# Performance work log

Hardware: AMD Instinct MI355X
Metric: run time of the kernel (lower is better)

The kernel has to match this reference:

```python
import jax, jax.numpy as jnp
import numpy as np

N = 65536   # collocation points
D = 2       # input dim
C = 16      # num subdomains / partitions (4x4 grid)
PH = 128    # PoU hidden dim
PNMID = 2   # PoU middle (residual) layers: depth=4 -> 2 middle
SW = 256    # subnet width
SNMID = 2   # subnet middle layers: eqx MLP depth=3 -> 2 width->width layers


def setup_inputs() -> dict:
    key = jax.random.key(0)
    ks = jax.random.split(key, 8)

    def w(k, shape, fan_in):
        return jax.random.normal(k, shape, jnp.float32) / jnp.sqrt(jnp.float32(fan_in))

    x = jax.random.uniform(ks[0], (N, D), jnp.float32)  # points in [0,1]^2
    # 4x4 grid of axis-aligned subdomains covering [0,1]^2
    g = np.linspace(0.0, 1.0, 5)
    lo = np.stack(np.meshgrid(g[:-1], g[:-1], indexing='ij'), -1).reshape(-1, 2)
    hi = np.stack(np.meshgrid(g[1:], g[1:], indexing='ij'), -1).reshape(-1, 2)
    centers = jnp.asarray((lo + hi) / 2.0, jnp.float32)  # [C, D]
    scales = jnp.asarray((hi - lo) / 2.0, jnp.float32)   # [C, D]

    return dict(
        x=x, centers=centers, scales=scales,
        pou_W0=w(ks[1], (D, PH), D), pou_b0=jnp.zeros((PH,), jnp.float32),
        pou_Wmid=w(ks[2], (PNMID, PH, PH), PH), pou_bmid=jnp.zeros((PNMID, PH), jnp.float32),
        pou_Wl=w(ks[3], (PH, C), PH), pou_bl=jnp.zeros((C,), jnp.float32),
        sub_W0=w(ks[4], (C, D, SW), D), sub_b0=jnp.zeros((C, SW), jnp.float32),
        sub_Wmid=w(ks[5], (C, SNMID, SW, SW), SW), sub_bmid=jnp.zeros((C, SNMID, SW), jnp.float32),
        sub_Wl=w(ks[6], (C, SW, 1), SW), sub_bl=jnp.zeros((C, 1), jnp.float32),
    )


def reference(x, centers, scales,
              pou_W0, pou_b0, pou_Wmid, pou_bmid, pou_Wl, pou_bl,
              sub_W0, sub_b0, sub_Wmid, sub_bmid, sub_Wl, sub_bl):
    # --- PoU gating net: residual ReLU MLP + softmax over partitions ---
    h = jax.nn.relu(x @ pou_W0 + pou_b0)                  # [N, PH]
    for l in range(pou_Wmid.shape[0]):
        h = h + jax.nn.relu(h @ pou_Wmid[l] + pou_bmid[l])
    wgt = jax.nn.softmax(h @ pou_Wl + pou_bl, axis=-1)    # [N, C] window weights

    # --- per-subdomain input normalization + batched subnet MLPs (tanh) ---
    xn = (x[None, :, :] - centers[:, None, :]) / scales[:, None, :]  # [C, N, D]
    g = jnp.tanh(jnp.einsum('cnd,cdw->cnw', xn, sub_W0) + sub_b0[:, None, :])  # [C, N, SW]
    for l in range(sub_Wmid.shape[1]):
        g = jnp.tanh(jnp.einsum('cnw,cwv->cnv', g, sub_Wmid[:, l]) + sub_bmid[:, l][:, None, :])
    u = (jnp.einsum('cnw,cwo->cno', g, sub_Wl) + sub_bl[:, None, :])[:, :, 0]  # [C, N]

    # --- windowed weighted sum:  acc_n = sum_c w[n,c] * u[c,n] ---
    acc = jnp.einsum('nc,cn->n', wgt, u)                  # [N]

    # --- ansatz: hard Dirichlet BC on the unit box: u = acc * prod_d x_d (1-x_d) ---
    return acc * jnp.prod(x * (1.0 - x), axis=-1)
```

## Files before the change

### kernel.cpp

```cpp
#include <hip/hip_runtime.h>

#define NPTS 65536
#define CC 16
#define PH 128
#define SW 256
#define MB 64
#define SP 264
#define TS 2.8853900817779268f

typedef _Float16 half8 __attribute__((ext_vector_type(8)));
typedef _Float16 half4 __attribute__((ext_vector_type(4)));
typedef _Float16 half2 __attribute__((ext_vector_type(2)));
typedef float float4_ __attribute__((ext_vector_type(4)));
typedef float float2_ __attribute__((ext_vector_type(2)));
typedef unsigned int uint2_ __attribute__((ext_vector_type(2)));

__device__ __forceinline__ float tanh_e(float y) {
    float e = __builtin_amdgcn_exp2f(y);
    float r = __builtin_amdgcn_rcpf(e + 1.0f);
    return fmaf(-2.0f, r, 1.0f);
}

__device__ __forceinline__ void store_pk4(_Float16* p, float a, float b, float c, float d) {
    uint2_ u;
    u.x = __builtin_bit_cast(unsigned int, __builtin_amdgcn_cvt_pkrtz(a, b));
    u.y = __builtin_bit_cast(unsigned int, __builtin_amdgcn_cvt_pkrtz(c, d));
    *(uint2_*)p = u;
}

__global__ __launch_bounds__(256) void prep_wt(const float* __restrict__ Wmid,
                                               _Float16* __restrict__ Wt) {
    __shared__ float T[64][65];
    int b = blockIdx.x;
    int cl = b >> 4;
    int tile = b & 15;
    int w0 = (tile >> 2) * 64, v0 = (tile & 3) * 64;
    int t = threadIdx.x;
    int col = t & 63, row4 = t >> 6;
    const float* src = Wmid + ((size_t)cl << 16);
#pragma unroll
    for (int rr = 0; rr < 16; ++rr) {
        int wl = rr * 4 + row4;
        T[wl][col] = src[(size_t)(w0 + wl) * 256 + v0 + col];
    }
    __syncthreads();
    _Float16* dst = Wt + ((size_t)cl << 16);
#pragma unroll
    for (int rr = 0; rr < 16; ++rr) {
        int v = rr * 4 + row4;
        dst[(size_t)(v0 + v) * 256 + w0 + col] = (_Float16)(T[col][v] * TS);
    }
}

__global__ __launch_bounds__(256) void pou_kernel(
    const float* __restrict__ x, const float* __restrict__ W0,
    const float* __restrict__ b0, const float* __restrict__ Wmid,
    const float* __restrict__ bmid, const float* __restrict__ Wl,
    const float* __restrict__ bl, float* __restrict__ wgtT) {
    __shared__ float hA[64][PH + 1];
    int t = threadIdx.x;
    int p = t & 63;
    int g4 = __builtin_amdgcn_readfirstlane(t >> 6);
    int jb = g4 * 32;
    int n0 = blockIdx.x * 64;
    float x0 = x[(size_t)(n0 + p) * 2];
    float x1 = x[(size_t)(n0 + p) * 2 + 1];

#pragma unroll
    for (int jj = 0; jj < 32; ++jj) {
        int j = jb + jj;
        float a = x0 * W0[j] + x1 * W0[PH + j] + b0[j];
        hA[p][j] = a > 0.f ? a : 0.f;
    }
    __syncthreads();

    for (int l = 0; l < 2; ++l) {
        float acc[32];
#pragma unroll
        for (int jj = 0; jj < 32; ++jj) acc[jj] = bmid[l * PH + jb + jj];
        for (int k = 0; k < PH; ++k) {
            float hv = hA[p][k];
#pragma unroll
            for (int jj = 0; jj < 32; ++jj)
                acc[jj] += hv * Wmid[(l * PH + k) * PH + jb + jj];
        }
        float resv[32];
#pragma unroll
        for (int jj = 0; jj < 32; ++jj) resv[jj] = hA[p][jb + jj];
        __syncthreads();
#pragma unroll
        for (int jj = 0; jj < 32; ++jj) {
            float r = acc[jj] > 0.f ? acc[jj] : 0.f;
            hA[p][jb + jj] = resv[jj] + r;
        }
        __syncthreads();
    }

    int c4 = g4 * 4;
    float lacc[4];
#pragma unroll
    for (int cc = 0; cc < 4; ++cc) lacc[cc] = bl[c4 + cc];
    for (int k = 0; k < PH; ++k) {
        float hv = hA[p][k];
#pragma unroll
        for (int cc = 0; cc < 4; ++cc) lacc[cc] += hv * Wl[k * CC + c4 + cc];
    }
    __syncthreads();
#pragma unroll
    for (int cc = 0; cc < 4; ++cc) hA[p][c4 + cc] = lacc[cc];
    __syncthreads();

    if (t < 64) {
        float lg[CC];
#pragma unroll
        for (int c = 0; c < CC; ++c) lg[c] = hA[t][c];
        float m = lg[0];
#pragma unroll
        for (int c = 1; c < CC; ++c) m = fmaxf(m, lg[c]);
        float s = 0.f;
#pragma unroll
        for (int c = 0; c < CC; ++c) {
            lg[c] = __builtin_amdgcn_exp2f((lg[c] - m) * 1.4426950408889634f);
            s += lg[c];
        }
        float inv = 1.0f / s;
#pragma unroll
        for (int c = 0; c < CC; ++c)
            wgtT[(size_t)c * NPTS + n0 + t] = lg[c] * inv;
    }
}

__global__ __launch_bounds__(256, 4) void subnet_kernel(
    const float* __restrict__ x, const float* __restrict__ centers,
    const float* __restrict__ scales, const float* __restrict__ W0,
    const float* __restrict__ b0, const _Float16* __restrict__ Wt,
    const float* __restrict__ bmid, const float* __restrict__ Wl,
    const float* __restrict__ bl, const float* __restrict__ wgtT,
    float* __restrict__ out) {
    __shared__ _Float16 g[MB * SP];
    __shared__ float part[4][MB];
    int t = threadIdx.x;
    int c = blockIdx.y;
    int n0 = blockIdx.x * MB;

    {
        float cx0 = centers[c * 2], cx1 = centers[c * 2 + 1];
        float is0 = 1.0f / scales[c * 2], is1 = 1.0f / scales[c * 2 + 1];
        int ln = t & 63;
        int pb = (t >> 6) * 16;
        const float* W0c = W0 + (size_t)c * 2 * SW;
        float4_ w0 = *(const float4_*)&W0c[ln * 4];
        float4_ w1 = *(const float4_*)&W0c[SW + ln * 4];
        float4_ bb = *(const float4_*)&b0[c * SW + ln * 4];
        w0 *= TS; w1 *= TS; bb *= TS;
#pragma unroll 4
        for (int p = 0; p < 16; ++p) {
            float2_ xv = *(const float2_*)&x[(size_t)(n0 + pb + p) * 2];
            float xn0 = (xv[0] - cx0) * is0;
            float xn1 = (xv[1] - cx1) * is1;
            float tv[4];
#pragma unroll
            for (int j = 0; j < 4; ++j)
                tv[j] = tanh_e(fmaf(xn0, w0[j], fmaf(xn1, w1[j], bb[j])));
            store_pk4(&g[(pb + p) * SP + ln * 4], tv[0], tv[1], tv[2], tv[3]);
        }
    }
    __syncthreads();

    int lane = t & 63;
    int wave = t >> 6;
    int quad = lane >> 4;
    int l16 = lane & 15;
    int mb = wave * 64;

    {
        const _Float16* Wp = Wt + (((size_t)(c * 2 + 0)) << 16);
        const _Float16* Arow = Wp + (mb + l16) * SW + quad * 8;
        const float* bp = bmid + (c * 2 + 0) * SW + mb + quad * 4;
        float4_ acc[4][4];
#pragma unroll
        for (int mt = 0; mt < 4; ++mt) {
            float4_ bv = *(const float4_*)&bp[mt * 16];
            bv *= TS;
#pragma unroll
            for (int nt = 0; nt < 4; ++nt) acc[mt][nt] = bv;
        }
        __builtin_amdgcn_s_setprio(1);
#pragma unroll
        for (int kt = 0; kt < 8; ++kt) {
            half8 a[4], b[4];
#pragma unroll
            for (int mt = 0; mt < 4; ++mt)
                a[mt] = *(const half8*)&Arow[mt * 16 * SW + kt * 32];
#pragma unroll
            for (int nt = 0; nt < 4; ++nt)
                b[nt] = *(const half8*)&g[(nt * 16 + l16) * SP + kt * 32 + quad * 8];
#pragma unroll
            for (int mt = 0; mt < 4; ++mt)
#pragma unroll
                for (int nt = 0; nt < 4; ++nt)
                    acc[mt][nt] = __builtin_amdgcn_mfma_f32_16x16x32_f16(
                        a[mt], b[nt], acc[mt][nt], 0, 0, 0);
        }
        __builtin_amdgcn_s_setprio(0);
#pragma unroll
        for (int mt = 0; mt < 4; ++mt)
#pragma unroll
            for (int nt = 0; nt < 4; ++nt) {
                acc[mt][nt][0] = tanh_e(acc[mt][nt][0]);
                acc[mt][nt][1] = tanh_e(acc[mt][nt][1]);
                acc[mt][nt][2] = tanh_e(acc[mt][nt][2]);
                acc[mt][nt][3] = tanh_e(acc[mt][nt][3]);
            }
        __syncthreads();
#pragma unroll
        for (int mt = 0; mt < 4; ++mt) {
#pragma unroll
            for (int nt = 0; nt < 4; ++nt) {
                store_pk4(&g[(nt * 16 + l16) * SP + mb + mt * 16 + quad * 4],
                          acc[mt][nt][0], acc[mt][nt][1],
                          acc[mt][nt][2], acc[mt][nt][3]);
            }
        }
        __syncthreads();
    }

    {
        const _Float16* Wp = Wt + (((size_t)(c * 2 + 1)) << 16);
        const _Float16* Arow = Wp + (mb + l16) * SW + quad * 8;
        const float* bp = bmid + (c * 2 + 1) * SW + mb + quad * 4;
        float4_ acc[4][4];
#pragma unroll
        for (int mt = 0; mt < 4; ++mt) {
            float4_ bv = *(const float4_*)&bp[mt * 16];
            bv *= TS;
#pragma unroll
            for (int nt = 0; nt < 4; ++nt) acc[mt][nt] = bv;
        }
        __builtin_amdgcn_s_setprio(1);
#pragma unroll
        for (int kt = 0; kt < 8; ++kt) {
            half8 a[4], b[4];
#pragma unroll
            for (int mt = 0; mt < 4; ++mt)
                a[mt] = *(const half8*)&Arow[mt * 16 * SW + kt * 32];
#pragma unroll
            for (int nt = 0; nt < 4; ++nt)
                b[nt] = *(const half8*)&g[(nt * 16 + l16) * SP + kt * 32 + quad * 8];
#pragma unroll
            for (int mt = 0; mt < 4; ++mt)
#pragma unroll
                for (int nt = 0; nt < 4; ++nt)
                    acc[mt][nt] = __builtin_amdgcn_mfma_f32_16x16x32_f16(
                        a[mt], b[nt], acc[mt][nt], 0, 0, 0);
        }
        __builtin_amdgcn_s_setprio(0);
        const float* wlp = Wl + c * SW + mb + quad * 4;
        float s[4] = {0.f, 0.f, 0.f, 0.f};
#pragma unroll
        for (int mt = 0; mt < 4; ++mt) {
            float4_ wv = *(const float4_*)&wlp[mt * 16];
#pragma unroll
            for (int nt = 0; nt < 4; ++nt) {
                float t0 = tanh_e(acc[mt][nt][0]);
                float t1 = tanh_e(acc[mt][nt][1]);
                float t2 = tanh_e(acc[mt][nt][2]);
                float t3 = tanh_e(acc[mt][nt][3]);
                s[nt] += fmaf(t0, wv[0],
                          fmaf(t1, wv[1], fmaf(t2, wv[2], t3 * wv[3])));
            }
        }
#pragma unroll
        for (int nt = 0; nt < 4; ++nt) {
            s[nt] += __shfl_xor(s[nt], 16);
            s[nt] += __shfl_xor(s[nt], 32);
        }
        if (quad == 0) {
#pragma unroll
            for (int nt = 0; nt < 4; ++nt) part[wave][nt * 16 + l16] = s[nt];
        }
    }
    __syncthreads();
    if (t < MB) {
        int n = n0 + t;
        float uv = part[0][t] + part[1][t] + part[2][t] + part[3][t] + bl[c];
        float w = wgtT[(size_t)c * NPTS + n];
        float2_ xv = *(const float2_*)&x[(size_t)n * 2];
        float ans = (xv[0] * (1.f - xv[0])) * (xv[1] * (1.f - xv[1]));
        atomicAdd(&out[n], uv * w * ans);
    }
}

extern "C" void kernel_launch(void* const* d_in, const int* in_sizes, int n_in,
                              void* d_out, int out_size, void* d_ws, size_t ws_size,
                              hipStream_t stream) {
    const float* x = (const float*)d_in[0];
    const float* centers = (const float*)d_in[1];
    const float* scales = (const float*)d_in[2];
    const float* pou_W0 = (const float*)d_in[3];
    const float* pou_b0 = (const float*)d_in[4];
    const float* pou_Wmid = (const float*)d_in[5];
    const float* pou_bmid = (const float*)d_in[6];
    const float* pou_Wl = (const float*)d_in[7];
    const float* pou_bl = (const float*)d_in[8];
    const float* sub_W0 = (const float*)d_in[9];
    const float* sub_b0 = (const float*)d_in[10];
    const float* sub_Wmid = (const float*)d_in[11];
    const float* sub_bmid = (const float*)d_in[12];
    const float* sub_Wl = (const float*)d_in[13];
    const float* sub_bl = (const float*)d_in[14];
    float* out = (float*)d_out;

    _Float16* wt = (_Float16*)d_ws;
    float* wgtT = (float*)((char*)d_ws + (4u << 20));

    hipMemsetAsync(out, 0, (size_t)out_size * sizeof(float), stream);
    prep_wt<<<dim3(512), dim3(256), 0, stream>>>(sub_Wmid, wt);
    pou_kernel<<<dim3(NPTS / 64), dim3(256), 0, stream>>>(
        x, pou_W0, pou_b0, pou_Wmid, pou_bmid, pou_Wl, pou_bl, wgtT);
    subnet_kernel<<<dim3(NPTS / MB, CC), dim3(256), 0, stream>>>(
        x, centers, scales, sub_W0, sub_b0, wt, sub_bmid, sub_Wl, sub_bl,
        wgtT, out);
}
```

Baseline: 660.4 us.

## Split subnet MFMA tiles into halves, XOR-swizzle LDS, raise occupancy to 5 waves

Each wave's 64-row output tile is now computed in two 32-row halves. This shrinks live accumulator registers so launch bounds can request 5 blocks per CU instead of 4. The padded LDS row stride is replaced by an XOR swizzle, which drops the padding and lets the partial-sum buffer alias the activation buffer, cutting shared memory per block. The s_setprio hints are removed. In exchange, the B operands are reloaded from LDS once per half, and the packed intermediate results must be held until the barrier.

```diff
diff --git a/kernel.cpp b/kernel.cpp
--- a/kernel.cpp
+++ b/kernel.cpp
@@ -5,7 +5,6 @@
 #define PH 128
 #define SW 256
 #define MB 64
-#define SP 264
 #define TS 2.8853900817779268f
 
 typedef _Float16 half8 __attribute__((ext_vector_type(8)));
@@ -21,11 +20,15 @@
     return fmaf(-2.0f, r, 1.0f);
 }
 
-__device__ __forceinline__ void store_pk4(_Float16* p, float a, float b, float c, float d) {
+__device__ __forceinline__ uint2_ pk4(float a, float b, float c, float d) {
     uint2_ u;
     u.x = __builtin_bit_cast(unsigned int, __builtin_amdgcn_cvt_pkrtz(a, b));
     u.y = __builtin_bit_cast(unsigned int, __builtin_amdgcn_cvt_pkrtz(c, d));
-    *(uint2_*)p = u;
+    return u;
+}
+
+__device__ __forceinline__ int swz(int row, int col_h) {
+    return row * 256 + (col_h ^ ((row & 7) << 3));
 }
 
 __global__ __launch_bounds__(256) void prep_wt(const float* __restrict__ Wmid,
@@ -130,15 +133,14 @@
     }
 }
 
-__global__ __launch_bounds__(256, 4) void subnet_kernel(
+__global__ __launch_bounds__(256, 5) void subnet_kernel(
     const float* __restrict__ x, const float* __restrict__ centers,
     const float* __restrict__ scales, const float* __restrict__ W0,
     const float* __restrict__ b0, const _Float16* __restrict__ Wt,
     const float* __restrict__ bmid, const float* __restrict__ Wl,
     const float* __restrict__ bl, const float* __restrict__ wgtT,
     float* __restrict__ out) {
-    __shared__ _Float16 g[MB * SP];
-    __shared__ float part[4][MB];
+    __shared__ _Float16 g[MB * 256];
     int t = threadIdx.x;
     int c = blockIdx.y;
     int n0 = blockIdx.x * MB;
@@ -162,7 +164,7 @@
 #pragma unroll
             for (int j = 0; j < 4; ++j)
                 tv[j] = tanh_e(fmaf(xn0, w0[j], fmaf(xn1, w1[j], bb[j])));
-            store_pk4(&g[(pb + p) * SP + ln * 4], tv[0], tv[1], tv[2], tv[3]);
+            *(uint2_*)&g[swz(pb + p, ln * 4)] = pk4(tv[0], tv[1], tv[2], tv[3]);
         }
     }
     __syncthreads();
@@ -174,116 +176,118 @@
     int mb = wave * 64;
 
     {
+        uint2_ pk[2][2][4];
         const _Float16* Wp = Wt + (((size_t)(c * 2 + 0)) << 16);
-        const _Float16* Arow = Wp + (mb + l16) * SW + quad * 8;
-        const float* bp = bmid + (c * 2 + 0) * SW + mb + quad * 4;
-        float4_ acc[4][4];
-#pragma unroll
-        for (int mt = 0; mt < 4; ++mt) {
-            float4_ bv = *(const float4_*)&bp[mt * 16];
-            bv *= TS;
-#pragma unroll
-            for (int nt = 0; nt < 4; ++nt) acc[mt][nt] = bv;
-        }
-        __builtin_amdgcn_s_setprio(1);
-#pragma unroll
-        for (int kt = 0; kt < 8; ++kt) {
-            half8 a[4], b[4];
-#pragma unroll
-            for (int mt = 0; mt < 4; ++mt)
-                a[mt] = *(const half8*)&Arow[mt * 16 * SW + kt * 32];
-#pragma unroll
-            for (int nt = 0; nt < 4; ++nt)
-                b[nt] = *(const half8*)&g[(nt * 16 + l16) * SP + kt * 32 + quad * 8];
-#pragma unroll
-            for (int mt = 0; mt < 4; ++mt)
+#pragma unroll
+        for (int mh = 0; mh < 2; ++mh) {
+            const _Float16* Arow = Wp + (mb + mh * 32 + l16) * SW + quad * 8;
+            const float* bp = bmid + (c * 2 + 0) * SW + mb + mh * 32 + quad * 4;
+            float4_ acc[2][4];
+#pragma unroll
+            for (int mt = 0; mt < 2; ++mt) {
+                float4_ bv = *(const float4_*)&bp[mt * 16];
+                bv *= TS;
+#pragma unroll
+                for (int nt = 0; nt < 4; ++nt) acc[mt][nt] = bv;
+            }
+#pragma unroll
+            for (int kt = 0; kt < 8; ++kt) {
+                half8 a[2], b[4];
+#pragma unroll
+                for (int mt = 0; mt < 2; ++mt)
+                    a[mt] = *(const half8*)&Arow[mt * 16 * SW + kt * 32];
 #pragma unroll
                 for (int nt = 0; nt < 4; ++nt)
-                    acc[mt][nt] = __builtin_amdgcn_mfma_f32_16x16x32_f16(
-                        a[mt], b[nt], acc[mt][nt], 0, 0, 0);
-        }
-        __builtin_amdgcn_s_setprio(0);
-#pragma unroll
-        for (int mt = 0; mt < 4; ++mt)
-#pragma unroll
-            for (int nt = 0; nt < 4; ++nt) {
-                acc[mt][nt][0] = tanh_e(acc[mt][nt][0]);
-                acc[mt][nt][1] = tanh_e(acc[mt][nt][1]);
-                acc[mt][nt][2] = tanh_e(acc[mt][nt][2]);
-                acc[mt][nt][3] = tanh_e(acc[mt][nt][3]);
-            }
+                    b[nt] = *(const half8*)&g[swz(nt * 16 + l16, kt * 32 + quad * 8)];
+#pragma unroll
+                for (int mt = 0; mt < 2; ++mt)
+#pragma unroll
+                    for (int nt = 0; nt < 4; ++nt)
+                        acc[mt][nt] = __builtin_amdgcn_mfma_f32_16x16x32_f16(
+                            a[mt], b[nt], acc[mt][nt], 0, 0, 0);
+            }
+#pragma unroll
+            for (int mt = 0; mt < 2; ++mt)
+#pragma unroll
+                for (int nt = 0; nt < 4; ++nt)
+                    pk[mh][mt][nt] = pk4(tanh_e(acc[mt][nt][0]), tanh_e(acc[mt][nt][1]),
+                                         tanh_e(acc[mt][nt][2]), tanh_e(acc[mt][nt][3]));
+        }
         __syncthreads();
 #pragma unroll
-        for (int mt = 0; mt < 4; ++mt) {
-#pragma unroll
-            for (int nt = 0; nt < 4; ++nt) {
-                store_pk4(&g[(nt * 16 + l16) * SP + mb + mt * 16 + quad * 4],
-                          acc[mt][nt][0], acc[mt][nt][1],
-                          acc[mt][nt][2], acc[mt][nt][3]);
-            }
-        }
+        for (int mh = 0; mh < 2; ++mh)
+#pragma unroll
+            for (int mt = 0; mt < 2; ++mt)
+#pragma unroll
+                for (int nt = 0; nt < 4; ++nt)
+                    *(uint2_*)&g[swz(nt * 16 + l16, mb + mh * 32 + mt * 16 + quad * 4)] =
+                        pk[mh][mt][nt];
         __syncthreads();
     }
 
+    float s[4] = {0.f, 0.f, 0.f, 0.f};
     {
         const _Float16* Wp = Wt + (((size_t)(c * 2 + 1)) << 16);
-        const _Float16* Arow = Wp + (mb + l16) * SW + quad * 8;
-        const float* bp = bmid + (c * 2 + 1) * SW + mb + quad * 4;
-        float4_ acc[4][4];
-#pragma unroll
-        for (int mt = 0; mt < 4; ++mt) {
-            float4_ bv = *(const float4_*)&bp[mt * 16];
-            bv *= TS;
-#pragma unroll
-            for (int nt = 0; nt < 4; ++nt) acc[mt][nt] = bv;
-        }
-        __builtin_amdgcn_s_setprio(1);
-#pragma unroll
-        for (int kt = 0; kt < 8; ++kt) {
-            half8 a[4], b[4];
-#pragma unroll
-            for (int mt = 0; mt < 4; ++mt)
-                a[mt] = *(const half8*)&Arow[mt * 16 * SW + kt * 32];
-#pragma unroll
-            for (int nt = 0; nt < 4; ++nt)
-                b[nt] = *(const half8*)&g[(nt * 16 + l16) * SP + kt * 32 + quad * 8];
-#pragma unroll
-            for (int mt = 0; mt < 4; ++mt)
+#pragma unroll
+        for (int mh = 0; mh < 2; ++mh) {
+            const _Float16* Arow = Wp + (mb + mh * 32 + l16) * SW + quad * 8;
+            const float* bp = bmid + (c * 2 + 1) * SW + mb + mh * 32 + quad * 4;
+            float4_ acc[2][4];
+#pragma unroll
+            for (int mt = 0; mt < 2; ++mt) {
+                float4_ bv = *(const float4_*)&bp[mt * 16];
+                bv *= TS;
+#pragma unroll
+                for (int nt = 0; nt < 4; ++nt) acc[mt][nt] = bv;
+            }
+#pragma unroll
+            for (int kt = 0; kt < 8; ++kt) {
+                half8 a[2], b[4];
+#pragma unroll
+                for (int mt = 0; mt < 2; ++mt)
+                    a[mt] = *(const half8*)&Arow[mt * 16 * SW + kt * 32];
 #pragma unroll
                 for (int nt = 0; nt < 4; ++nt)
-                    acc[mt][nt] = __builtin_amdgcn_mfma_f32_16x16x32_f16(
-                        a[mt], b[nt], acc[mt][nt], 0, 0, 0);
-        }
-        __builtin_amdgcn_s_setprio(0);
-        const float* wlp = Wl + c * SW + mb + quad * 4;
-        float s[4] = {0.f, 0.f, 0.f, 0.f};
-#pragma unroll
-        for (int mt = 0; mt < 4; ++mt) {
-            float4_ wv = *(const float4_*)&wlp[mt * 16];
-#pragma unroll
-            for (int nt = 0; nt < 4; ++nt) {
-                float t0 = tanh_e(acc[mt][nt][0]);
-                float t1 = tanh_e(acc[mt][nt][1]);
-                float t2 = tanh_e(acc[mt][nt][2]);
-                float t3 = tanh_e(acc[mt][nt][3]);
-                s[nt] += fmaf(t0, wv[0],
-                          fmaf(t1, wv[1], fmaf(t2, wv[2], t3 * wv[3])));
-            }
-        }
-#pragma unroll
-        for (int nt = 0; nt < 4; ++nt) {
-            s[nt] += __shfl_xor(s[nt], 16);
-            s[nt] += __shfl_xor(s[nt], 32);
-        }
-        if (quad == 0) {
-#pragma unroll
-            for (int nt = 0; nt < 4; ++nt) part[wave][nt * 16 + l16] = s[nt];
-        }
+                    b[nt] = *(const half8*)&g[swz(nt * 16 + l16, kt * 32 + quad * 8)];
+#pragma unroll
+                for (int mt = 0; mt < 2; ++mt)
+#pragma unroll
+                    for (int nt = 0; nt < 4; ++nt)
+                        acc[mt][nt] = __builtin_amdgcn_mfma_f32_16x16x32_f16(
+                            a[mt], b[nt], acc[mt][nt], 0, 0, 0);
+            }
+            const float* wlp = Wl + c * SW + mb + mh * 32 + quad * 4;
+#pragma unroll
+            for (int mt = 0; mt < 2; ++mt) {
+                float4_ wv = *(const float4_*)&wlp[mt * 16];
+#pragma unroll
+                for (int nt = 0; nt < 4; ++nt) {
+                    float t0 = tanh_e(acc[mt][nt][0]);
+                    float t1 = tanh_e(acc[mt][nt][1]);
+                    float t2 = tanh_e(acc[mt][nt][2]);
+                    float t3 = tanh_e(acc[mt][nt][3]);
+                    s[nt] += fmaf(t0, wv[0],
+                              fmaf(t1, wv[1], fmaf(t2, wv[2], t3 * wv[3])));
+                }
+            }
+        }
+    }
+#pragma unroll
+    for (int nt = 0; nt < 4; ++nt) {
+        s[nt] += __shfl_xor(s[nt], 16);
+        s[nt] += __shfl_xor(s[nt], 32);
+    }
+    __syncthreads();
+    float* part = (float*)g;
+    if (quad == 0) {
+#pragma unroll
+        for (int nt = 0; nt < 4; ++nt) part[wave * 64 + nt * 16 + l16] = s[nt];
     }
     __syncthreads();
     if (t < MB) {
         int n = n0 + t;
-        float uv = part[0][t] + part[1][t] + part[2][t] + part[3][t] + bl[c];
+        float uv = part[0 * 64 + t] + part[1 * 64 + t] + part[2 * 64 + t] +
+                   part[3 * 64 + t] + bl[c];
         float w = wgtT[(size_t)c * NPTS + n];
         float2_ xv = *(const float2_*)&x[(size_t)n * 2];
         float ans = (xv[0] * (1.f - xv[0])) * (xv[1] * (1.f - xv[1]));
```

Result: slower. 969.0 us (+46.7%).

## Loop over subdomains inside each block, dropping atomics and output memset

Applied to the files above, without the earlier changes.

The subnet kernel is now launched over point tiles only, and each block iterates over all 16 subdomains with a staggered starting index. It accumulates the weighted sum in a register and writes the output directly. This removes the hipMemsetAsync, the 16-way atomicAdd contention per point and the repeated final epilogue. The cost is that the grid shrinks from 16384 to 1024 blocks, which lowers available parallelism and latency hiding. The s_setprio hints are also dropped, and the part buffer is now reused across iterations, which needs the extra barriers.

```diff
diff --git a/kernel.cpp b/kernel.cpp
--- a/kernel.cpp
+++ b/kernel.cpp
@@ -21,11 +21,11 @@
     return fmaf(-2.0f, r, 1.0f);
 }
 
-__device__ __forceinline__ void store_pk4(_Float16* p, float a, float b, float c, float d) {
+__device__ __forceinline__ uint2_ pk4(float a, float b, float c, float d) {
     uint2_ u;
     u.x = __builtin_bit_cast(unsigned int, __builtin_amdgcn_cvt_pkrtz(a, b));
     u.y = __builtin_bit_cast(unsigned int, __builtin_amdgcn_cvt_pkrtz(c, d));
-    *(uint2_*)p = u;
+    return u;
 }
 
 __global__ __launch_bounds__(256) void prep_wt(const float* __restrict__ Wmid,
@@ -140,134 +140,134 @@
     __shared__ _Float16 g[MB * SP];
     __shared__ float part[4][MB];
     int t = threadIdx.x;
-    int c = blockIdx.y;
     int n0 = blockIdx.x * MB;
-
-    {
-        float cx0 = centers[c * 2], cx1 = centers[c * 2 + 1];
-        float is0 = 1.0f / scales[c * 2], is1 = 1.0f / scales[c * 2 + 1];
-        int ln = t & 63;
-        int pb = (t >> 6) * 16;
-        const float* W0c = W0 + (size_t)c * 2 * SW;
-        float4_ w0 = *(const float4_*)&W0c[ln * 4];
-        float4_ w1 = *(const float4_*)&W0c[SW + ln * 4];
-        float4_ bb = *(const float4_*)&b0[c * SW + ln * 4];
-        w0 *= TS; w1 *= TS; bb *= TS;
-#pragma unroll 4
-        for (int p = 0; p < 16; ++p) {
-            float2_ xv = *(const float2_*)&x[(size_t)(n0 + pb + p) * 2];
-            float xn0 = (xv[0] - cx0) * is0;
-            float xn1 = (xv[1] - cx1) * is1;
-            float tv[4];
-#pragma unroll
-            for (int j = 0; j < 4; ++j)
-                tv[j] = tanh_e(fmaf(xn0, w0[j], fmaf(xn1, w1[j], bb[j])));
-            store_pk4(&g[(pb + p) * SP + ln * 4], tv[0], tv[1], tv[2], tv[3]);
-        }
-    }
-    __syncthreads();
 
     int lane = t & 63;
     int wave = t >> 6;
     int quad = lane >> 4;
     int l16 = lane & 15;
     int mb = wave * 64;
-
-    {
-        const _Float16* Wp = Wt + (((size_t)(c * 2 + 0)) << 16);
-        const _Float16* Arow = Wp + (mb + l16) * SW + quad * 8;
-        const float* bp = bmid + (c * 2 + 0) * SW + mb + quad * 4;
-        float4_ acc[4][4];
-#pragma unroll
-        for (int mt = 0; mt < 4; ++mt) {
-            float4_ bv = *(const float4_*)&bp[mt * 16];
-            bv *= TS;
-#pragma unroll
-            for (int nt = 0; nt < 4; ++nt) acc[mt][nt] = bv;
-        }
-        __builtin_amdgcn_s_setprio(1);
-#pragma unroll
-        for (int kt = 0; kt < 8; ++kt) {
-            half8 a[4], b[4];
+    int ln = t & 63;
+    int pb = (t >> 6) * 16;
+
+    float uacc = 0.f;
+    int c0 = blockIdx.x & 15;
+
+    for (int ci = 0; ci < CC; ++ci) {
+        int c = (c0 + ci) & 15;
+
+        {
+            float cx0 = centers[c * 2], cx1 = centers[c * 2 + 1];
+            float is0 = 1.0f / scales[c * 2], is1 = 1.0f / scales[c * 2 + 1];
+            const float* W0c = W0 + (size_t)c * 2 * SW;
+            float4_ w0 = *(const float4_*)&W0c[ln * 4];
+            float4_ w1 = *(const float4_*)&W0c[SW + ln * 4];
+            float4_ bb = *(const float4_*)&b0[c * SW + ln * 4];
+            w0 *= TS; w1 *= TS; bb *= TS;
+#pragma unroll 4
+            for (int p = 0; p < 16; ++p) {
+                float2_ xv = *(const float2_*)&x[(size_t)(n0 + pb + p) * 2];
+                float xn0 = (xv[0] - cx0) * is0;
+                float xn1 = (xv[1] - cx1) * is1;
+                float tv[4];
+#pragma unroll
+                for (int j = 0; j < 4; ++j)
+                    tv[j] = tanh_e(fmaf(xn0, w0[j], fmaf(xn1, w1[j], bb[j])));
+                *(uint2_*)&g[(pb + p) * SP + ln * 4] = pk4(tv[0], tv[1], tv[2], tv[3]);
+            }
+        }
+        __syncthreads();
+
+        {
+            const _Float16* Wp = Wt + (((size_t)(c * 2 + 0)) << 16);
+            const _Float16* Arow = Wp + (mb + l16) * SW + quad * 8;
+            const float* bp = bmid + (c * 2 + 0) * SW + mb + quad * 4;
+            float4_ acc[4][4];
+#pragma unroll
+            for (int mt = 0; mt < 4; ++mt) {
+                float4_ bv = *(const float4_*)&bp[mt * 16];
+                bv *= TS;
+#pragma unroll
+                for (int nt = 0; nt < 4; ++nt) acc[mt][nt] = bv;
+            }
+#pragma unroll
+            for (int kt = 0; kt < 8; ++kt) {
+                half8 a[4], b[4];
+#pragma unroll
+                for (int mt = 0; mt < 4; ++mt)
+                    a[mt] = *(const half8*)&Arow[mt * 16 * SW + kt * 32];
+#pragma unroll
+                for (int nt = 0; nt < 4; ++nt)
+                    b[nt] = *(const half8*)&g[(nt * 16 + l16) * SP + kt * 32 + quad * 8];
+#pragma unroll
+                for (int mt = 0; mt < 4; ++mt)
+#pragma unroll
+                    for (int nt = 0; nt < 4; ++nt)
+                        acc[mt][nt] = __builtin_amdgcn_mfma_f32_16x16x32_f16(
+                            a[mt], b[nt], acc[mt][nt], 0, 0, 0);
+            }
 #pragma unroll
             for (int mt = 0; mt < 4; ++mt)
-                a[mt] = *(const half8*)&Arow[mt * 16 * SW + kt * 32];
-#pragma unroll
-            for (int nt = 0; nt < 4; ++nt)
-                b[nt] = *(const half8*)&g[(nt * 16 + l16) * SP + kt * 32 + quad * 8];
+#pragma unroll
+                for (int nt = 0; nt < 4; ++nt) {
+                    acc[mt][nt][0] = tanh_e(acc[mt][nt][0]);
+                    acc[mt][nt][1] = tanh_e(acc[mt][nt][1]);
+                    acc[mt][nt][2] = tanh_e(acc[mt][nt][2]);
+                    acc[mt][nt][3] = tanh_e(acc[mt][nt][3]);
+                }
+            __syncthreads();
 #pragma unroll
             for (int mt = 0; mt < 4; ++mt)
 #pragma unroll
                 for (int nt = 0; nt < 4; ++nt)
-                    acc[mt][nt] = __builtin_amdgcn_mfma_f32_16x16x32_f16(
-                        a[mt], b[nt], acc[mt][nt], 0, 0, 0);
-        }
-        __builtin_amdgcn_s_setprio(0);
-#pragma unroll
-        for (int mt = 0; mt < 4; ++mt)
-#pragma unroll
-            for (int nt = 0; nt < 4; ++nt) {
-                acc[mt][nt][0] = tanh_e(acc[mt][nt][0]);
-                acc[mt][nt][1] = tanh_e(acc[mt][nt][1]);
-                acc[mt][nt][2] = tanh_e(acc[mt][nt][2]);
-                acc[mt][nt][3] = tanh_e(acc[mt][nt][3]);
-            }
-        __syncthreads();
-#pragma unroll
-        for (int mt = 0; mt < 4; ++mt) {
-#pragma unroll
-            for (int nt = 0; nt < 4; ++nt) {
-                store_pk4(&g[(nt * 16 + l16) * SP + mb + mt * 16 + quad * 4],
-                          acc[mt][nt][0], acc[mt][nt][1],
-                          acc[mt][nt][2], acc[mt][nt][3]);
-            }
-        }
-        __syncthreads();
-    }
-
-    {
-        const _Float16* Wp = Wt + (((size_t)(c * 2 + 1)) << 16);
-        const _Float16* Arow = Wp + (mb + l16) * SW + quad * 8;
-        const float* bp = bmid + (c * 2 + 1) * SW + mb + quad * 4;
-        float4_ acc[4][4];
-#pragma unroll
-        for (int mt = 0; mt < 4; ++mt) {
-            float4_ bv = *(const float4_*)&bp[mt * 16];
-            bv *= TS;
-#pragma unroll
-            for (int nt = 0; nt < 4; ++nt) acc[mt][nt] = bv;
-        }
-        __builtin_amdgcn_s_setprio(1);
-#pragma unroll
-        for (int kt = 0; kt < 8; ++kt) {
-            half8 a[4], b[4];
-#pragma unroll
-            for (int mt = 0; mt < 4; ++mt)
-                a[mt] = *(const half8*)&Arow[mt * 16 * SW + kt * 32];
-#pragma unroll
-            for (int nt = 0; nt < 4; ++nt)
-                b[nt] = *(const half8*)&g[(nt * 16 + l16) * SP + kt * 32 + quad * 8];
-#pragma unroll
-            for (int mt = 0; mt < 4; ++mt)
+                    *(uint2_*)&g[(nt * 16 + l16) * SP + mb + mt * 16 + quad * 4] =
+                        pk4(acc[mt][nt][0], acc[mt][nt][1],
+                            acc[mt][nt][2], acc[mt][nt][3]);
+            __syncthreads();
+        }
+
+        float s[4] = {0.f, 0.f, 0.f, 0.f};
+        {
+            const _Float16* Wp = Wt + (((size_t)(c * 2 + 1)) << 16);
+            const _Float16* Arow = Wp + (mb + l16) * SW + quad * 8;
+            const float* bp = bmid + (c * 2 + 1) * SW + mb + quad * 4;
+            float4_ acc[4][4];
+#pragma unroll
+            for (int mt = 0; mt < 4; ++mt) {
+                float4_ bv = *(const float4_*)&bp[mt * 16];
+                bv *= TS;
+#pragma unroll
+                for (int nt = 0; nt < 4; ++nt) acc[mt][nt] = bv;
+            }
+#pragma unroll
+            for (int kt = 0; kt < 8; ++kt) {
+                half8 a[4], b[4];
+#pragma unroll
+                for (int mt = 0; mt < 4; ++mt)
+                    a[mt] = *(const half8*)&Arow[mt * 16 * SW + kt * 32];
 #pragma unroll
                 for (int nt = 0; nt < 4; ++nt)
-                    acc[mt][nt] = __builtin_amdgcn_mfma_f32_16x16x32_f16(
-                        a[mt], b[nt], acc[mt][nt], 0, 0, 0);
-        }
-        __builtin_amdgcn_s_setprio(0);
-        const float* wlp = Wl + c * SW + mb + quad * 4;
-        float s[4] = {0.f, 0.f, 0.f, 0.f};
-#pragma unroll
-        for (int mt = 0; mt < 4; ++mt) {
-            float4_ wv = *(const float4_*)&wlp[mt * 16];
-#pragma unroll
-            for (int nt = 0; nt < 4; ++nt) {
-                float t0 = tanh_e(acc[mt][nt][0]);
-                float t1 = tanh_e(acc[mt][nt][1]);
-                float t2 = tanh_e(acc[mt][nt][2]);
-                float t3 = tanh_e(acc[mt][nt][3]);
-                s[nt] += fmaf(t0, wv[0],
-                          fmaf(t1, wv[1], fmaf(t2, wv[2], t3 * wv[3])));
+                    b[nt] = *(const half8*)&g[(nt * 16 + l16) * SP + kt * 32 + quad * 8];
+#pragma unroll
+                for (int mt = 0; mt < 4; ++mt)
+#pragma unroll
+                    for (int nt = 0; nt < 4; ++nt)
+                        acc[mt][nt] = __builtin_amdgcn_mfma_f32_16x16x32_f16(
+                            a[mt], b[nt], acc[mt][nt], 0, 0, 0);
+            }
+            const float* wlp = Wl + c * SW + mb + quad * 4;
+#pragma unroll
+            for (int mt = 0; mt < 4; ++mt) {
+                float4_ wv = *(const float4_*)&wlp[mt * 16];
+#pragma unroll
+                for (int nt = 0; nt < 4; ++nt) {
+                    float t0 = tanh_e(acc[mt][nt][0]);
+                    float t1 = tanh_e(acc[mt][nt][1]);
+                    float t2 = tanh_e(acc[mt][nt][2]);
+                    float t3 = tanh_e(acc[mt][nt][3]);
+                    s[nt] += fmaf(t0, wv[0],
+                              fmaf(t1, wv[1], fmaf(t2, wv[2], t3 * wv[3])));
+                }
             }
         }
 #pragma unroll
@@ -279,15 +279,18 @@
 #pragma unroll
             for (int nt = 0; nt < 4; ++nt) part[wave][nt * 16 + l16] = s[nt];
         }
-    }
-    __syncthreads();
+        __syncthreads();
+        if (t < MB) {
+            float uv = part[0][t] + part[1][t] + part[2][t] + part[3][t] + bl[c];
+            uacc = fmaf(uv, wgtT[(size_t)c * NPTS + n0 + t], uacc);
+        }
+    }
+
     if (t < MB) {
         int n = n0 + t;
-        float uv = part[0][t] + part[1][t] + part[2][t] + part[3][t] + bl[c];
-        float w = wgtT[(size_t)c * NPTS + n];
         float2_ xv = *(const float2_*)&x[(size_t)n * 2];
         float ans = (xv[0] * (1.f - xv[0])) * (xv[1] * (1.f - xv[1]));
-        atomicAdd(&out[n], uv * w * ans);
+        out[n] = uacc * ans;
     }
 }
 
@@ -314,11 +317,10 @@
     _Float16* wt = (_Float16*)d_ws;
     float* wgtT = (float*)((char*)d_ws + (4u << 20));
 
-    hipMemsetAsync(out, 0, (size_t)out_size * sizeof(float), stream);
     prep_wt<<<dim3(512), dim3(256), 0, stream>>>(sub_Wmid, wt);
     pou_kernel<<<dim3(NPTS / 64), dim3(256), 0, stream>>>(
         x, pou_W0, pou_b0, pou_Wmid, pou_bmid, pou_Wl, pou_bl, wgtT);
-    subnet_kernel<<<dim3(NPTS / MB, CC), dim3(256), 0, stream>>>(
+    subnet_kernel<<<dim3(NPTS / MB), dim3(256), 0, stream>>>(
         x, centers, scales, sub_W0, sub_b0, wt, sub_bmid, sub_Wl, sub_bl,
         wgtT, out);
 }
```

New measurement: 687.5 us. 4.1% more time.
